# Kernel tuning notes

Measured on AMD Instinct MI355X. Metric: run time of the kernel, lower is better.

Reference implementation:

```python
import jax, jax.numpy as jnp
import numpy as np

S, B, H, F, E, K = 2048, 4, 1024, 4096, 8, 2


def setup_inputs() -> dict:
    key = jax.random.key(0)
    k1, k2, k3, k4 = jax.random.split(key, 4)
    scale_h = 1.0 / np.sqrt(H)
    scale_f = 1.0 / np.sqrt(F)
    return {
        "x": jax.random.normal(k1, (S, B, H), dtype=jnp.float32),
        "router_w": jax.random.normal(k2, (H, E), dtype=jnp.float32) * scale_h,
        "w1": jax.random.normal(k3, (E, H, F), dtype=jnp.float32) * scale_h,
        "w2": jax.random.normal(k4, (E, F, H), dtype=jnp.float32) * scale_f,
    }


def reference(x, router_w, w1, w2):
    # x: [S, B, H] (Megatron layout). Flatten to tokens.
    s, b, h = x.shape
    xt = x.reshape(-1, h)                       # [T, H], T = S*B
    # --- TopK router: softmax over expert logits, then top-k probs ---
    logits = xt @ router_w                      # [T, E]
    probs = jax.nn.softmax(logits, axis=-1)     # [T, E]
    top_p, top_i = jax.lax.top_k(probs, K)      # [T, K] each
    # --- Grouped-GEMM expert MLPs + weighted combine ---
    # Loop over the small fixed expert set; each expert applies fc1->gelu->fc2
    # to every token, masked/weighted by its routing probability (math is
    # identical to dispatch/permute/grouped-GEMM/combine in Megatron).
    out = jnp.zeros_like(xt)
    for e in range(E):
        gate_e = jnp.sum(jnp.where(top_i == e, top_p, 0.0), axis=-1)  # [T]
        hidden = jax.nn.gelu(xt @ w1[e], approximate=True)            # [T, F]
        out = out + gate_e[:, None] * (hidden @ w2[e])                # [T, H]
    return out.reshape(s, b, h)
```

## Files before the change

kernel.cpp:

```cpp
#include <hip/hip_runtime.h>
#include <cstdint>
#include <cstddef>

#define T_TOKENS 8192
#define H_DIM    1024
#define F_DIM    4096
#define E_NUM    8

typedef __bf16 bf16x8 __attribute__((ext_vector_type(8)));
typedef float  f32x4  __attribute__((ext_vector_type(4)));
typedef unsigned short ushort8 __attribute__((ext_vector_type(8)));

#define AS_GLOBAL(p) ((const __attribute__((address_space(1))) void*)(p))
#define AS_LDS(p)    ((__attribute__((address_space(3))) void*)(p))

__device__ inline unsigned short f2b(float f) {
  unsigned int u = __float_as_uint(f);
  unsigned int r = (u + 0x7fffu + ((u >> 16) & 1u)) >> 16;
  return (unsigned short)r;
}
__device__ inline float b2f(unsigned short u) {
  return __uint_as_float(((unsigned int)u) << 16);
}
__device__ inline float gelu_fast(float v) {
  float u2 = 1.5957691216057308f * v * (1.0f + 0.044715f * v * v);
  return v / (1.0f + __expf(-u2));
}

__global__ __launch_bounds__(256) void transpose_cast_kernel(
    const float* __restrict__ in, unsigned short* __restrict__ out, int R, int C,
    int* __restrict__ zc)
{
  __shared__ float tile[64][65];
  const int tid = threadIdx.x;
  if (zc && blockIdx.x == 0 && blockIdx.y == 0 && blockIdx.z == 0 && tid < 24)
    zc[tid] = 0;
  const int e  = blockIdx.z;
  const int c0 = blockIdx.x * 64;
  const int r0 = blockIdx.y * 64;
  const float* src = in + (size_t)e * R * C;
  unsigned short* dst = out + (size_t)e * R * C;
  const int rl  = tid >> 4;
  const int cl4 = (tid & 15) * 4;
#pragma unroll
  for (int i = 0; i < 4; ++i) {
    float4 v = *(const float4*)(src + (size_t)(r0 + rl + i * 16) * C + c0 + cl4);
    tile[rl + i * 16][cl4 + 0] = v.x;
    tile[rl + i * 16][cl4 + 1] = v.y;
    tile[rl + i * 16][cl4 + 2] = v.z;
    tile[rl + i * 16][cl4 + 3] = v.w;
  }
  __syncthreads();
#pragma unroll
  for (int itw = 0; itw < 2; ++itw) {
    int g  = itw * 256 + tid;
    int c  = g >> 3;
    int rc = g & 7;
    ushort8 u;
#pragma unroll
    for (int k = 0; k < 8; ++k) u[k] = f2b(tile[rc * 8 + k][c]);
    *(ushort8*)(dst + (size_t)(c0 + c) * R + r0 + rc * 8) = u;
  }
}

__global__ __launch_bounds__(256) void router_kernel(
    const float* __restrict__ x, const float* __restrict__ rw,
    unsigned short* __restrict__ xb, int* __restrict__ top_e, float* __restrict__ top_p,
    int* __restrict__ counts, float* __restrict__ out_zero)
{
  __shared__ float lrw[H_DIM * 9];
  __shared__ int lc[E_NUM];
  const int tid = threadIdx.x;
  {
    float4 z = {0.f, 0.f, 0.f, 0.f};
    float4* o4 = (float4*)out_zero;
    int base = blockIdx.x * 256 + tid;
#pragma unroll
    for (int i = 0; i < 32; ++i) o4[base + i * 65536] = z;
  }
  if (tid < E_NUM) lc[tid] = 0;
  for (int r = tid; r < H_DIM; r += 256) {
    const float* s = rw + r * 8;
    float4 a = *(const float4*)(s);
    float4 b = *(const float4*)(s + 4);
    float* d = &lrw[r * 9];
    d[0] = a.x; d[1] = a.y; d[2] = a.z; d[3] = a.w;
    d[4] = b.x; d[5] = b.y; d[6] = b.z; d[7] = b.w;
  }
  __syncthreads();
  const int lane = tid & 63, wid = tid >> 6;
  for (int i = 0; i < 8; ++i) {
    const int t = blockIdx.x * 32 + wid * 8 + i;
    float acc[8] = {0.f, 0.f, 0.f, 0.f, 0.f, 0.f, 0.f, 0.f};
    const float* xrow = x + (size_t)t * H_DIM;
    unsigned short* xbrow = xb + (size_t)t * H_DIM;
#pragma unroll
    for (int j = 0; j < 16; ++j) {
      int h = j * 64 + lane;
      float xv = xrow[h];
      xbrow[h] = f2b(xv);
      const float* rr = &lrw[h * 9];
#pragma unroll
      for (int e = 0; e < 8; ++e) acc[e] += xv * rr[e];
    }
#pragma unroll
    for (int e = 0; e < 8; ++e) {
#pragma unroll
      for (int s = 32; s > 0; s >>= 1) acc[e] += __shfl_xor(acc[e], s, 64);
    }
    if (lane == 0) {
      float mx = acc[0];
      for (int e = 1; e < 8; ++e) mx = fmaxf(mx, acc[e]);
      float p[8]; float sum = 0.f;
      for (int e = 0; e < 8; ++e) { p[e] = expf(acc[e] - mx); sum += p[e]; }
      float inv = 1.0f / sum;
      int i1 = 0; float b1 = p[0];
      for (int e = 1; e < 8; ++e) if (p[e] > b1) { b1 = p[e]; i1 = e; }
      int i2 = (i1 == 0) ? 1 : 0; float b2 = p[i2];
      for (int e = 0; e < 8; ++e) if (e != i1 && p[e] > b2) { b2 = p[e]; i2 = e; }
      top_e[2 * t]     = i1; top_p[2 * t]     = b1 * inv;
      top_e[2 * t + 1] = i2; top_p[2 * t + 1] = b2 * inv;
      atomicAdd(&lc[i1], 1);
      atomicAdd(&lc[i2], 1);
    }
  }
  __syncthreads();
  if (tid < E_NUM) atomicAdd(&counts[tid], lc[tid]);
}

__global__ __launch_bounds__(256) void assign_kernel(
    const int* __restrict__ top_e, const float* __restrict__ top_p,
    const int* __restrict__ counts, int* __restrict__ cursor,
    int* __restrict__ map, float* __restrict__ gate, int* __restrict__ offsets)
{
  __shared__ int lc[E_NUM], lb[E_NUM], loff[E_NUM];
  const int tid = threadIdx.x;
  const int t = blockIdx.x * 256 + tid;
  if (tid < E_NUM) lc[tid] = 0;
  if (tid == 0) {
    int o = 0;
    for (int e = 0; e < E_NUM; ++e) { loff[e] = o; o += counts[e]; }
  }
  __syncthreads();
  int e0 = top_e[2 * t], e1 = top_e[2 * t + 1];
  int p0 = atomicAdd(&lc[e0], 1);
  int p1 = atomicAdd(&lc[e1], 1);
  __syncthreads();
  if (tid < E_NUM) lb[tid] = atomicAdd(&cursor[tid], lc[tid]);
  __syncthreads();
  int s0 = loff[e0] + lb[e0] + p0;
  int s1 = loff[e1] + lb[e1] + p1;
  map[s0] = t; gate[s0] = top_p[2 * t];
  map[s1] = t; gate[s1] = top_p[2 * t + 1];
  if (blockIdx.x == 0 && tid < E_NUM) offsets[tid] = loff[tid];
}

template <int KD, int ND, bool USE_MAP, bool GELU, bool ATOMIC_OUT>
__global__ __launch_bounds__(256) void moe_gemm_kernel(
    const unsigned short* __restrict__ A, const unsigned short* __restrict__ Bt,
    const int* __restrict__ map, const float* __restrict__ gate,
    const int* __restrict__ counts, const int* __restrict__ offsets,
    unsigned short* __restrict__ C, float* __restrict__ out)
{
  __shared__ unsigned short ls[32768];
  const int e   = blockIdx.x;
  const int cnt = counts[e];
  const int tile_m = blockIdx.y;
  if (tile_m * 128 >= cnt) return;
  const int off    = offsets[e];
  const int tile_n = blockIdx.z;
  const int tid    = threadIdx.x;

  const unsigned short* aSrc[4];
  const unsigned short* bSrc[4];
  const int cswz = ((tid & 7) ^ ((tid >> 3) & 7)) * 8;
#pragma unroll
  for (int it = 0; it < 4; ++it) {
    int r  = it * 32 + (tid >> 3);
    int rm = tile_m * 128 + r;
    if (rm > cnt - 1) rm = cnt - 1;
    int arow = USE_MAP ? map[off + rm] : (off + rm);
    aSrc[it] = A + (size_t)arow * KD + cswz;
    int rn = tile_n * 128 + r;
    bSrc[it] = Bt + (size_t)e * ND * KD + (size_t)rn * KD + cswz;
  }

  const int lane = tid & 63;
  const int wid  = tid >> 6;
  const int wm = wid >> 1, wn = wid & 1;
  const int lr = lane & 15, kg = lane >> 4;
  const int swz = lr & 7;

  f32x4 acc[4][4];
#pragma unroll
  for (int mi = 0; mi < 4; ++mi)
#pragma unroll
    for (int ni = 0; ni < 4; ++ni) acc[mi][ni] = (f32x4){0.f, 0.f, 0.f, 0.f};

  constexpr int NK = KD / 64;

#pragma unroll
  for (int it = 0; it < 4; ++it)
    __builtin_amdgcn_global_load_lds(AS_GLOBAL(aSrc[it]),
                                     AS_LDS(ls + (it * 256 + tid) * 8), 16, 0, 0);
#pragma unroll
  for (int it = 0; it < 4; ++it)
    __builtin_amdgcn_global_load_lds(AS_GLOBAL(bSrc[it]),
                                     AS_LDS(ls + 16384 + (it * 256 + tid) * 8), 16, 0, 0);

#pragma unroll 1
  for (int k = 0; k < NK; ++k) {
    const int p = k & 1;
    asm volatile("s_barrier" ::: "memory");
    if (k + 1 < NK) {
      const int q = p ^ 1;
      const int k0 = (k + 1) * 64;
#pragma unroll
      for (int it = 0; it < 4; ++it)
        __builtin_amdgcn_global_load_lds(AS_GLOBAL(aSrc[it] + k0),
                                         AS_LDS(ls + q * 8192 + (it * 256 + tid) * 8), 16, 0, 0);
#pragma unroll
      for (int it = 0; it < 4; ++it)
        __builtin_amdgcn_global_load_lds(AS_GLOBAL(bSrc[it] + k0),
                                         AS_LDS(ls + 16384 + q * 8192 + (it * 256 + tid) * 8), 16, 0, 0);
      asm volatile("s_waitcnt vmcnt(8)" ::: "memory");
    } else {
      asm volatile("s_waitcnt vmcnt(0)" ::: "memory");
    }
    asm volatile("s_barrier" ::: "memory");

    const unsigned short* pA = ls + p * 8192 + (wm * 64 + lr) * 64;
    const unsigned short* pB = ls + 16384 + p * 8192 + (wn * 64 + lr) * 64;
#pragma unroll
    for (int ks = 0; ks < 2; ++ks) {
      bf16x8 aF[4], bF[4];
#pragma unroll
      for (int i = 0; i < 4; ++i)
        aF[i] = *(const bf16x8*)(pA + i * 16 * 64 + (((ks * 4 + kg) ^ swz) * 8));
#pragma unroll
      for (int i = 0; i < 4; ++i)
        bF[i] = *(const bf16x8*)(pB + i * 16 * 64 + (((ks * 4 + kg) ^ swz) * 8));
#pragma unroll
      for (int mi = 0; mi < 4; ++mi)
#pragma unroll
        for (int ni = 0; ni < 4; ++ni)
          acc[mi][ni] = __builtin_amdgcn_mfma_f32_16x16x32_bf16(aF[mi], bF[ni],
                                                                acc[mi][ni], 0, 0, 0);
    }
  }

  if (ATOMIC_OUT) {
#pragma unroll
    for (int mi = 0; mi < 4; ++mi) {
#pragma unroll
      for (int r = 0; r < 4; ++r) {
        int Rl = wm * 64 + mi * 16 + kg * 4 + r;
        int gm = tile_m * 128 + Rl;
        if (gm < cnt) {
          int   t  = map[off + gm];
          float gv = gate[off + gm];
          float* orow = out + (size_t)t * ND + tile_n * 128 + wn * 64 + lr;
#pragma unroll
          for (int ni = 0; ni < 4; ++ni)
            __hip_atomic_fetch_add(orow + ni * 16, acc[mi][ni][r] * gv,
                                   __ATOMIC_RELAXED, __HIP_MEMORY_SCOPE_AGENT);
        }
      }
    }
  } else {
    __syncthreads();
#pragma unroll
    for (int mi = 0; mi < 4; ++mi) {
#pragma unroll
      for (int r = 0; r < 4; ++r) {
        int Rl = wm * 64 + mi * 16 + kg * 4 + r;
#pragma unroll
        for (int ni = 0; ni < 4; ++ni) {
          int col = wn * 64 + ni * 16 + lr;
          float v = acc[mi][ni][r];
          v = GELU ? gelu_fast(v) : v;
          ls[Rl * 136 + col] = f2b(v);
        }
      }
    }
    __syncthreads();
#pragma unroll
    for (int it = 0; it < 8; ++it) {
      int g = it * 256 + tid;
      int R = g >> 4, c16 = g & 15;
      int gm = tile_m * 128 + R;
      if (gm < cnt) {
        ushort8 v = *(const ushort8*)(ls + R * 136 + c16 * 8);
        *(ushort8*)(C + (size_t)(off + gm) * ND + tile_n * 128 + c16 * 8) = v;
      }
    }
  }
}

extern "C" void kernel_launch(void* const* d_in, const int* in_sizes, int n_in,
                              void* d_out, int out_size, void* d_ws, size_t ws_size,
                              hipStream_t stream) {
  const float* x  = (const float*)d_in[0];
  const float* rw = (const float*)d_in[1];
  const float* w1 = (const float*)d_in[2];
  const float* w2 = (const float*)d_in[3];
  float* out = (float*)d_out;

  char* ws = (char*)d_ws;
  unsigned short* wT     = (unsigned short*)ws;
  unsigned short* xb     = (unsigned short*)(ws + (64ull  << 20));
  unsigned short* hidden = (unsigned short*)(ws + (96ull  << 20));
  char* meta = ws + (224ull << 20);
  int*   top_e   = (int*)meta;
  float* top_p   = (float*)(meta + (64 << 10));
  int*   map     = (int*)(meta + (128 << 10));
  float* gate    = (float*)(meta + (192 << 10));
  int*   counts  = (int*)(meta + (320 << 10));
  int*   offsets = counts + 8;
  int*   cursor  = counts + 16;

  transpose_cast_kernel<<<dim3(F_DIM / 64, H_DIM / 64, E_NUM), 256, 0, stream>>>(
      w1, wT, H_DIM, F_DIM, counts);
  router_kernel<<<256, 256, 0, stream>>>(x, rw, xb, top_e, top_p, counts, out);
  assign_kernel<<<T_TOKENS / 256, 256, 0, stream>>>(top_e, top_p, counts, cursor,
                                                    map, gate, offsets);
  moe_gemm_kernel<H_DIM, F_DIM, true, true, false>
      <<<dim3(E_NUM, 64, F_DIM / 128), 256, 0, stream>>>(xb, wT, map, gate,
                                                         counts, offsets, hidden, nullptr);
  transpose_cast_kernel<<<dim3(H_DIM / 64, F_DIM / 64, E_NUM), 256, 0, stream>>>(
      w2, wT, F_DIM, H_DIM, nullptr);
  moe_gemm_kernel<F_DIM, H_DIM, false, false, true>
      <<<dim3(E_NUM, 64, H_DIM / 128), 256, 0, stream>>>(hidden, wT, map, gate,
                                                         counts, offsets, nullptr, out);
}
```

Measured before the change: 765.1 us.

## Add 256x256-tile triple-buffered GEMM kernel for the fc1 expert stage

Adds a new grouped-GEMM kernel for fc1 that uses 512-thread blocks computing 256x256 output tiles with a k-step of 32. It keeps three LDS buffers filled through global_load_lds and splits the A/B staging between two MFMA phases, which raise wave priority via setprio. The aim is more data reuse per block and better overlap of loads with MFMA work than the older 128x128 kernel. The cost is 96KB of LDS and larger accumulator register use per block, which lowers occupancy and may leave tiles partly empty when an expert has few tokens.

```diff
diff --git a/kernel.cpp b/kernel.cpp
--- a/kernel.cpp
+++ b/kernel.cpp
@@ -155,6 +155,153 @@
   if (blockIdx.x == 0 && tid < E_NUM) offsets[tid] = loff[tid];
 }
 
+template <int KD, int ND, bool USE_MAP, bool GELU>
+__global__ __launch_bounds__(512, 2) void moe_gemm_k32_kernel(
+    const unsigned short* __restrict__ A, const unsigned short* __restrict__ Bt,
+    const int* __restrict__ map, const float* __restrict__ gate,
+    const int* __restrict__ counts, const int* __restrict__ offsets,
+    unsigned short* __restrict__ C)
+{
+  __shared__ unsigned short ls[49152];
+  const int e   = blockIdx.x;
+  const int cnt = counts[e];
+  const int tile_m = blockIdx.y;
+  if (tile_m * 256 >= cnt) return;
+  const int off    = offsets[e];
+  const int tile_n = blockIdx.z;
+  const int tid    = threadIdx.x;
+
+  const unsigned short* aSrc[2];
+  const unsigned short* bSrc[2];
+#pragma unroll
+  for (int it = 0; it < 2; ++it) {
+    int g   = it * 512 + tid;
+    int row = g >> 2;
+    int cs  = (g & 3) ^ (row & 3);
+    int rm  = tile_m * 256 + row;
+    if (rm > cnt - 1) rm = cnt - 1;
+    int arow = USE_MAP ? map[off + rm] : (off + rm);
+    aSrc[it] = A + (size_t)arow * KD + cs * 8;
+    int rn = tile_n * 256 + row;
+    bSrc[it] = Bt + (size_t)e * ND * KD + (size_t)rn * KD + cs * 8;
+  }
+
+  const int lane = tid & 63;
+  const int wid  = tid >> 6;
+  const int wm = wid >> 2, wn = wid & 3;
+  const int lr = lane & 15, kg = lane >> 4;
+  const int kc = ((kg ^ (lr & 3)) * 8);
+
+  f32x4 acc[8][4];
+#pragma unroll
+  for (int mi = 0; mi < 8; ++mi)
+#pragma unroll
+    for (int ni = 0; ni < 4; ++ni) acc[mi][ni] = (f32x4){0.f, 0.f, 0.f, 0.f};
+
+  constexpr int NK = KD / 32;
+
+  auto STAGE_A = [&](int kt, int slot) {
+    const int kof = kt * 32;
+#pragma unroll
+    for (int it = 0; it < 2; ++it)
+      __builtin_amdgcn_global_load_lds(AS_GLOBAL(aSrc[it] + kof),
+          AS_LDS(ls + slot * 8192 + (it * 512 + tid) * 8), 16, 0, 0);
+  };
+  auto STAGE_B = [&](int kt, int slot) {
+    const int kof = kt * 32;
+#pragma unroll
+    for (int it = 0; it < 2; ++it)
+      __builtin_amdgcn_global_load_lds(AS_GLOBAL(bSrc[it] + kof),
+          AS_LDS(ls + 24576 + slot * 8192 + (it * 512 + tid) * 8), 16, 0, 0);
+  };
+
+  STAGE_A(0, 0); STAGE_B(0, 0);
+  STAGE_A(1, 1); STAGE_B(1, 1);
+  asm volatile("s_waitcnt vmcnt(4)" ::: "memory");
+  asm volatile("s_barrier" ::: "memory");
+
+  int sc = 0;
+  int st = 2;
+#pragma unroll 1
+  for (int kt = 0; kt < NK; ++kt) {
+    const bool stg = (kt + 2 < NK);
+    const unsigned short* pA = ls + sc * 8192 + (wm * 128 + lr) * 32;
+    const unsigned short* pB = ls + 24576 + sc * 8192 + (wn * 64 + lr) * 32;
+    bf16x8 aF[4], bF[4];
+
+#pragma unroll
+    for (int ni = 0; ni < 4; ++ni)
+      bF[ni] = *(const bf16x8*)(pB + ni * 16 * 32 + kc);
+#pragma unroll
+    for (int j = 0; j < 4; ++j)
+      aF[j] = *(const bf16x8*)(pA + j * 16 * 32 + kc);
+    if (stg) STAGE_A(kt + 2, st);
+    asm volatile("s_barrier" ::: "memory");
+    __builtin_amdgcn_s_setprio(1);
+#pragma unroll
+    for (int j = 0; j < 4; ++j)
+#pragma unroll
+      for (int ni = 0; ni < 4; ++ni)
+        acc[j][ni] = __builtin_amdgcn_mfma_f32_16x16x32_bf16(aF[j], bF[ni], acc[j][ni], 0, 0, 0);
+    __builtin_amdgcn_s_setprio(0);
+    asm volatile("s_barrier" ::: "memory");
+
+#pragma unroll
+    for (int j = 0; j < 4; ++j)
+      aF[j] = *(const bf16x8*)(pA + (4 + j) * 16 * 32 + kc);
+    if (stg) STAGE_B(kt + 2, st);
+    asm volatile("s_barrier" ::: "memory");
+    __builtin_amdgcn_s_setprio(1);
+#pragma unroll
+    for (int j = 0; j < 4; ++j)
+#pragma unroll
+      for (int ni = 0; ni < 4; ++ni)
+        acc[4 + j][ni] = __builtin_amdgcn_mfma_f32_16x16x32_bf16(aF[j], bF[ni], acc[4 + j][ni], 0, 0, 0);
+    __builtin_amdgcn_s_setprio(0);
+    if (stg) {
+      asm volatile("s_waitcnt vmcnt(4)" ::: "memory");
+    } else if (kt + 1 < NK) {
+      asm volatile("s_waitcnt vmcnt(0)" ::: "memory");
+    }
+    asm volatile("s_barrier" ::: "memory");
+    sc = (sc == 2) ? 0 : sc + 1;
+    st = (st == 2) ? 0 : st + 1;
+  }
+
+  __syncthreads();
+#pragma unroll
+  for (int h = 0; h < 2; ++h) {
+    if (h) __syncthreads();
+    if (wm == h) {
+#pragma unroll
+      for (int mi = 0; mi < 8; ++mi) {
+#pragma unroll
+        for (int r = 0; r < 4; ++r) {
+          int Rl = mi * 16 + kg * 4 + r;
+#pragma unroll
+          for (int ni = 0; ni < 4; ++ni) {
+            int col = wn * 64 + ni * 16 + lr;
+            float v = acc[mi][ni][r];
+            v = GELU ? gelu_fast(v) : v;
+            ls[Rl * 264 + col] = f2b(v);
+          }
+        }
+      }
+    }
+    __syncthreads();
+#pragma unroll
+    for (int it = 0; it < 8; ++it) {
+      int g = it * 512 + tid;
+      int R = g >> 5, c8 = g & 31;
+      int gm = tile_m * 256 + h * 128 + R;
+      if (gm < cnt) {
+        ushort8 v = *(const ushort8*)(ls + R * 264 + c8 * 8);
+        *(ushort8*)(C + (size_t)(off + gm) * ND + tile_n * 256 + c8 * 8) = v;
+      }
+    }
+  }
+}
+
 template <int KD, int ND, bool USE_MAP, bool GELU, bool ATOMIC_OUT>
 __global__ __launch_bounds__(256) void moe_gemm_kernel(
     const unsigned short* __restrict__ A, const unsigned short* __restrict__ Bt,
@@ -324,9 +471,9 @@
   router_kernel<<<256, 256, 0, stream>>>(x, rw, xb, top_e, top_p, counts, out);
   assign_kernel<<<T_TOKENS / 256, 256, 0, stream>>>(top_e, top_p, counts, cursor,
                                                     map, gate, offsets);
-  moe_gemm_kernel<H_DIM, F_DIM, true, true, false>
-      <<<dim3(E_NUM, 64, F_DIM / 128), 256, 0, stream>>>(xb, wT, map, gate,
-                                                         counts, offsets, hidden, nullptr);
+  moe_gemm_k32_kernel<H_DIM, F_DIM, true, true>
+      <<<dim3(E_NUM, 32, F_DIM / 256), 512, 0, stream>>>(xb, wT, map, gate,
+                                                         counts, offsets, hidden);
   transpose_cast_kernel<<<dim3(H_DIM / 64, F_DIM / 64, E_NUM), 256, 0, stream>>>(
       w2, wT, F_DIM, H_DIM, nullptr);
   moe_gemm_kernel<F_DIM, H_DIM, false, false, true>
```

Result: slower. 826.1 us (+8.0%).

## Replace atomic scatter-add combine with per-slot gated output and gather combine

Applied to the files above, without the earlier changes.

The second expert GEMM now writes gate-weighted results as bf16 rows per routed slot instead of doing fp32 atomic adds into the output. A new combine kernel gathers each token's two slot rows via a slot_of index built in the assign kernel and writes the fp32 sum, so the output zeroing in the router is dropped. This removes contended global atomics and the zero-fill pass. In exchange it adds an extra kernel and an intermediate buffer, and rounds per-expert contributions to bf16 before summing.

```diff
diff --git a/kernel.cpp b/kernel.cpp
--- a/kernel.cpp
+++ b/kernel.cpp
@@ -66,18 +66,11 @@
 __global__ __launch_bounds__(256) void router_kernel(
     const float* __restrict__ x, const float* __restrict__ rw,
     unsigned short* __restrict__ xb, int* __restrict__ top_e, float* __restrict__ top_p,
-    int* __restrict__ counts, float* __restrict__ out_zero)
+    int* __restrict__ counts)
 {
   __shared__ float lrw[H_DIM * 9];
   __shared__ int lc[E_NUM];
   const int tid = threadIdx.x;
-  {
-    float4 z = {0.f, 0.f, 0.f, 0.f};
-    float4* o4 = (float4*)out_zero;
-    int base = blockIdx.x * 256 + tid;
-#pragma unroll
-    for (int i = 0; i < 32; ++i) o4[base + i * 65536] = z;
-  }
   if (tid < E_NUM) lc[tid] = 0;
   for (int r = tid; r < H_DIM; r += 256) {
     const float* s = rw + r * 8;
@@ -131,7 +124,8 @@
 __global__ __launch_bounds__(256) void assign_kernel(
     const int* __restrict__ top_e, const float* __restrict__ top_p,
     const int* __restrict__ counts, int* __restrict__ cursor,
-    int* __restrict__ map, float* __restrict__ gate, int* __restrict__ offsets)
+    int* __restrict__ map, float* __restrict__ gate, int* __restrict__ slot_of,
+    int* __restrict__ offsets)
 {
   __shared__ int lc[E_NUM], lb[E_NUM], loff[E_NUM];
   const int tid = threadIdx.x;
@@ -152,15 +146,16 @@
   int s1 = loff[e1] + lb[e1] + p1;
   map[s0] = t; gate[s0] = top_p[2 * t];
   map[s1] = t; gate[s1] = top_p[2 * t + 1];
+  slot_of[2 * t] = s0; slot_of[2 * t + 1] = s1;
   if (blockIdx.x == 0 && tid < E_NUM) offsets[tid] = loff[tid];
 }
 
-template <int KD, int ND, bool USE_MAP, bool GELU, bool ATOMIC_OUT>
+template <int KD, int ND, bool USE_MAP>
 __global__ __launch_bounds__(256) void moe_gemm_kernel(
     const unsigned short* __restrict__ A, const unsigned short* __restrict__ Bt,
-    const int* __restrict__ map, const float* __restrict__ gate,
+    const int* __restrict__ map,
     const int* __restrict__ counts, const int* __restrict__ offsets,
-    unsigned short* __restrict__ C, float* __restrict__ out)
+    unsigned short* __restrict__ C)
 {
   __shared__ unsigned short ls[32768];
   const int e   = blockIdx.x;
@@ -249,52 +244,169 @@
     }
   }
 
-  if (ATOMIC_OUT) {
-#pragma unroll
-    for (int mi = 0; mi < 4; ++mi) {
-#pragma unroll
-      for (int r = 0; r < 4; ++r) {
-        int Rl = wm * 64 + mi * 16 + kg * 4 + r;
-        int gm = tile_m * 128 + Rl;
-        if (gm < cnt) {
-          int   t  = map[off + gm];
-          float gv = gate[off + gm];
-          float* orow = out + (size_t)t * ND + tile_n * 128 + wn * 64 + lr;
-#pragma unroll
-          for (int ni = 0; ni < 4; ++ni)
-            __hip_atomic_fetch_add(orow + ni * 16, acc[mi][ni][r] * gv,
-                                   __ATOMIC_RELAXED, __HIP_MEMORY_SCOPE_AGENT);
-        }
+  __syncthreads();
+#pragma unroll
+  for (int mi = 0; mi < 4; ++mi) {
+#pragma unroll
+    for (int r = 0; r < 4; ++r) {
+      int Rl = wm * 64 + mi * 16 + kg * 4 + r;
+#pragma unroll
+      for (int ni = 0; ni < 4; ++ni) {
+        int col = wn * 64 + ni * 16 + lr;
+        ls[Rl * 136 + col] = f2b(gelu_fast(acc[mi][ni][r]));
       }
     }
-  } else {
-    __syncthreads();
-#pragma unroll
-    for (int mi = 0; mi < 4; ++mi) {
-#pragma unroll
-      for (int r = 0; r < 4; ++r) {
-        int Rl = wm * 64 + mi * 16 + kg * 4 + r;
-#pragma unroll
-        for (int ni = 0; ni < 4; ++ni) {
-          int col = wn * 64 + ni * 16 + lr;
-          float v = acc[mi][ni][r];
-          v = GELU ? gelu_fast(v) : v;
-          ls[Rl * 136 + col] = f2b(v);
-        }
+  }
+  __syncthreads();
+#pragma unroll
+  for (int it = 0; it < 8; ++it) {
+    int g = it * 256 + tid;
+    int R = g >> 4, c16 = g & 15;
+    int gm = tile_m * 128 + R;
+    if (gm < cnt) {
+      ushort8 v = *(const ushort8*)(ls + R * 136 + c16 * 8);
+      *(ushort8*)(C + (size_t)(off + gm) * ND + tile_n * 128 + c16 * 8) = v;
+    }
+  }
+}
+
+template <int KD, int ND>
+__global__ __launch_bounds__(256) void moe_gemm_fc2_kernel(
+    const unsigned short* __restrict__ A, const unsigned short* __restrict__ Bt,
+    const float* __restrict__ gate,
+    const int* __restrict__ counts, const int* __restrict__ offsets,
+    unsigned short* __restrict__ C)
+{
+  __shared__ unsigned short ls[32768];
+  const int e   = blockIdx.x;
+  const int cnt = counts[e];
+  const int tile_m = blockIdx.y;
+  if (tile_m * 128 >= cnt) return;
+  const int off    = offsets[e];
+  const int tile_n = blockIdx.z;
+  const int tid    = threadIdx.x;
+
+  const unsigned short* aSrc[4];
+  const unsigned short* bSrc[4];
+  const int cswz = ((tid & 7) ^ ((tid >> 3) & 7)) * 8;
+#pragma unroll
+  for (int it = 0; it < 4; ++it) {
+    int r  = it * 32 + (tid >> 3);
+    int rm = tile_m * 128 + r;
+    if (rm > cnt - 1) rm = cnt - 1;
+    aSrc[it] = A + (size_t)(off + rm) * KD + cswz;
+    int rn = tile_n * 128 + r;
+    bSrc[it] = Bt + (size_t)e * ND * KD + (size_t)rn * KD + cswz;
+  }
+
+  const int lane = tid & 63;
+  const int wid  = tid >> 6;
+  const int wm = wid >> 1, wn = wid & 1;
+  const int lr = lane & 15, kg = lane >> 4;
+  const int swz = lr & 7;
+
+  f32x4 acc[4][4];
+#pragma unroll
+  for (int mi = 0; mi < 4; ++mi)
+#pragma unroll
+    for (int ni = 0; ni < 4; ++ni) acc[mi][ni] = (f32x4){0.f, 0.f, 0.f, 0.f};
+
+  constexpr int NK = KD / 64;
+
+#pragma unroll
+  for (int it = 0; it < 4; ++it)
+    __builtin_amdgcn_global_load_lds(AS_GLOBAL(aSrc[it]),
+                                     AS_LDS(ls + (it * 256 + tid) * 8), 16, 0, 0);
+#pragma unroll
+  for (int it = 0; it < 4; ++it)
+    __builtin_amdgcn_global_load_lds(AS_GLOBAL(bSrc[it]),
+                                     AS_LDS(ls + 16384 + (it * 256 + tid) * 8), 16, 0, 0);
+
+#pragma unroll 1
+  for (int k = 0; k < NK; ++k) {
+    const int p = k & 1;
+    asm volatile("s_barrier" ::: "memory");
+    if (k + 1 < NK) {
+      const int q = p ^ 1;
+      const int k0 = (k + 1) * 64;
+#pragma unroll
+      for (int it = 0; it < 4; ++it)
+        __builtin_amdgcn_global_load_lds(AS_GLOBAL(aSrc[it] + k0),
+                                         AS_LDS(ls + q * 8192 + (it * 256 + tid) * 8), 16, 0, 0);
+#pragma unroll
+      for (int it = 0; it < 4; ++it)
+        __builtin_amdgcn_global_load_lds(AS_GLOBAL(bSrc[it] + k0),
+                                         AS_LDS(ls + 16384 + q * 8192 + (it * 256 + tid) * 8), 16, 0, 0);
+      asm volatile("s_waitcnt vmcnt(8)" ::: "memory");
+    } else {
+      asm volatile("s_waitcnt vmcnt(0)" ::: "memory");
+    }
+    asm volatile("s_barrier" ::: "memory");
+
+    const unsigned short* pA = ls + p * 8192 + (wm * 64 + lr) * 64;
+    const unsigned short* pB = ls + 16384 + p * 8192 + (wn * 64 + lr) * 64;
+#pragma unroll
+    for (int ks = 0; ks < 2; ++ks) {
+      bf16x8 aF[4], bF[4];
+#pragma unroll
+      for (int i = 0; i < 4; ++i)
+        aF[i] = *(const bf16x8*)(pA + i * 16 * 64 + (((ks * 4 + kg) ^ swz) * 8));
+#pragma unroll
+      for (int i = 0; i < 4; ++i)
+        bF[i] = *(const bf16x8*)(pB + i * 16 * 64 + (((ks * 4 + kg) ^ swz) * 8));
+#pragma unroll
+      for (int mi = 0; mi < 4; ++mi)
+#pragma unroll
+        for (int ni = 0; ni < 4; ++ni)
+          acc[mi][ni] = __builtin_amdgcn_mfma_f32_16x16x32_bf16(aF[mi], bF[ni],
+                                                                acc[mi][ni], 0, 0, 0);
+    }
+  }
+
+  __syncthreads();
+#pragma unroll
+  for (int mi = 0; mi < 4; ++mi) {
+#pragma unroll
+    for (int r = 0; r < 4; ++r) {
+      int Rl = wm * 64 + mi * 16 + kg * 4 + r;
+      int gm = tile_m * 128 + Rl;
+      int gmc = gm < cnt ? gm : cnt - 1;
+      float gv = gate[off + gmc];
+#pragma unroll
+      for (int ni = 0; ni < 4; ++ni) {
+        int col = wn * 64 + ni * 16 + lr;
+        ls[Rl * 136 + col] = f2b(acc[mi][ni][r] * gv);
       }
     }
-    __syncthreads();
-#pragma unroll
-    for (int it = 0; it < 8; ++it) {
-      int g = it * 256 + tid;
-      int R = g >> 4, c16 = g & 15;
-      int gm = tile_m * 128 + R;
-      if (gm < cnt) {
-        ushort8 v = *(const ushort8*)(ls + R * 136 + c16 * 8);
-        *(ushort8*)(C + (size_t)(off + gm) * ND + tile_n * 128 + c16 * 8) = v;
-      }
-    }
-  }
+  }
+  __syncthreads();
+#pragma unroll
+  for (int it = 0; it < 8; ++it) {
+    int g = it * 256 + tid;
+    int R = g >> 4, c16 = g & 15;
+    int gm = tile_m * 128 + R;
+    if (gm < cnt) {
+      ushort8 v = *(const ushort8*)(ls + R * 136 + c16 * 8);
+      *(ushort8*)(C + (size_t)(off + gm) * ND + tile_n * 128 + c16 * 8) = v;
+    }
+  }
+}
+
+__global__ __launch_bounds__(256) void combine_kernel(
+    const unsigned short* __restrict__ y, const int* __restrict__ slot_of,
+    float* __restrict__ out)
+{
+  const int t  = blockIdx.x;
+  const int h0 = threadIdx.x * 4;
+  const int s0 = slot_of[2 * t], s1 = slot_of[2 * t + 1];
+  ushort4 a = *(const ushort4*)(y + (size_t)s0 * H_DIM + h0);
+  ushort4 b = *(const ushort4*)(y + (size_t)s1 * H_DIM + h0);
+  float4 o;
+  o.x = b2f(a.x) + b2f(b.x);
+  o.y = b2f(a.y) + b2f(b.y);
+  o.z = b2f(a.z) + b2f(b.z);
+  o.w = b2f(a.w) + b2f(b.w);
+  *(float4*)(out + (size_t)t * H_DIM + h0) = o;
 }
 
 extern "C" void kernel_launch(void* const* d_in, const int* in_sizes, int n_in,
@@ -309,27 +421,30 @@
   char* ws = (char*)d_ws;
   unsigned short* wT     = (unsigned short*)ws;
   unsigned short* xb     = (unsigned short*)(ws + (64ull  << 20));
+  unsigned short* y      = (unsigned short*)(ws + (64ull  << 20));
   unsigned short* hidden = (unsigned short*)(ws + (96ull  << 20));
   char* meta = ws + (224ull << 20);
   int*   top_e   = (int*)meta;
   float* top_p   = (float*)(meta + (64 << 10));
   int*   map     = (int*)(meta + (128 << 10));
   float* gate    = (float*)(meta + (192 << 10));
+  int*   slot_of = (int*)(meta + (256 << 10));
   int*   counts  = (int*)(meta + (320 << 10));
   int*   offsets = counts + 8;
   int*   cursor  = counts + 16;
 
   transpose_cast_kernel<<<dim3(F_DIM / 64, H_DIM / 64, E_NUM), 256, 0, stream>>>(
       w1, wT, H_DIM, F_DIM, counts);
-  router_kernel<<<256, 256, 0, stream>>>(x, rw, xb, top_e, top_p, counts, out);
+  router_kernel<<<256, 256, 0, stream>>>(x, rw, xb, top_e, top_p, counts);
   assign_kernel<<<T_TOKENS / 256, 256, 0, stream>>>(top_e, top_p, counts, cursor,
-                                                    map, gate, offsets);
-  moe_gemm_kernel<H_DIM, F_DIM, true, true, false>
-      <<<dim3(E_NUM, 64, F_DIM / 128), 256, 0, stream>>>(xb, wT, map, gate,
-                                                         counts, offsets, hidden, nullptr);
+                                                    map, gate, slot_of, offsets);
+  moe_gemm_kernel<H_DIM, F_DIM, true>
+      <<<dim3(E_NUM, 64, F_DIM / 128), 256, 0, stream>>>(xb, wT, map,
+                                                         counts, offsets, hidden);
   transpose_cast_kernel<<<dim3(H_DIM / 64, F_DIM / 64, E_NUM), 256, 0, stream>>>(
       w2, wT, F_DIM, H_DIM, nullptr);
-  moe_gemm_kernel<F_DIM, H_DIM, false, false, true>
-      <<<dim3(E_NUM, 64, H_DIM / 128), 256, 0, stream>>>(hidden, wT, map, gate,
-                                                         counts, offsets, nullptr, out);
-}
+  moe_gemm_fc2_kernel<F_DIM, H_DIM>
+      <<<dim3(E_NUM, 64, H_DIM / 128), 256, 0, stream>>>(hidden, wT, gate,
+                                                         counts, offsets, y);
+  combine_kernel<<<T_TOKENS, 256, 0, stream>>>(y, slot_of, out);
+}
```

Measured after the change: 740.5 us. 1.03x faster.

## Use 256x256 GEMM tiles with finer pipeline and replace atomic scatter with combine

Applied to the files above, without the earlier changes.

Both expert GEMMs move from 128x128 tiles on 256 threads to 256x256 tiles on 512 threads. Each 64-wide k step is split into two 32-wide half-stages across a four-slot LDS ring, with setprio around the MFMA bursts to overlap loads with compute. The second GEMM now writes gated bf16 results into a per-slot buffer instead of doing fp32 atomics into the output. A new combine kernel sums each token's two slots, which also removes the output zeroing. The bigger tiles mean more M-padding waste for experts with uneven counts, more register pressure, and a bf16 rounding of the fc2 output before the sum.

```diff
diff --git a/kernel.cpp b/kernel.cpp
--- a/kernel.cpp
+++ b/kernel.cpp
@@ -66,18 +66,11 @@
 __global__ __launch_bounds__(256) void router_kernel(
     const float* __restrict__ x, const float* __restrict__ rw,
     unsigned short* __restrict__ xb, int* __restrict__ top_e, float* __restrict__ top_p,
-    int* __restrict__ counts, float* __restrict__ out_zero)
+    int* __restrict__ counts)
 {
   __shared__ float lrw[H_DIM * 9];
   __shared__ int lc[E_NUM];
   const int tid = threadIdx.x;
-  {
-    float4 z = {0.f, 0.f, 0.f, 0.f};
-    float4* o4 = (float4*)out_zero;
-    int base = blockIdx.x * 256 + tid;
-#pragma unroll
-    for (int i = 0; i < 32; ++i) o4[base + i * 65536] = z;
-  }
   if (tid < E_NUM) lc[tid] = 0;
   for (int r = tid; r < H_DIM; r += 256) {
     const float* s = rw + r * 8;
@@ -131,7 +124,8 @@
 __global__ __launch_bounds__(256) void assign_kernel(
     const int* __restrict__ top_e, const float* __restrict__ top_p,
     const int* __restrict__ counts, int* __restrict__ cursor,
-    int* __restrict__ map, float* __restrict__ gate, int* __restrict__ offsets)
+    int* __restrict__ map, float* __restrict__ gate, int* __restrict__ slot_of,
+    int* __restrict__ offsets)
 {
   __shared__ int lc[E_NUM], lb[E_NUM], loff[E_NUM];
   const int tid = threadIdx.x;
@@ -152,149 +146,197 @@
   int s1 = loff[e1] + lb[e1] + p1;
   map[s0] = t; gate[s0] = top_p[2 * t];
   map[s1] = t; gate[s1] = top_p[2 * t + 1];
+  slot_of[2 * t] = s0; slot_of[2 * t + 1] = s1;
   if (blockIdx.x == 0 && tid < E_NUM) offsets[tid] = loff[tid];
 }
 
-template <int KD, int ND, bool USE_MAP, bool GELU, bool ATOMIC_OUT>
-__global__ __launch_bounds__(256) void moe_gemm_kernel(
+template <int KD, int ND, bool USE_MAP, bool GELU>
+__global__ __launch_bounds__(512, 2) void moe_gemm256_kernel(
     const unsigned short* __restrict__ A, const unsigned short* __restrict__ Bt,
     const int* __restrict__ map, const float* __restrict__ gate,
     const int* __restrict__ counts, const int* __restrict__ offsets,
-    unsigned short* __restrict__ C, float* __restrict__ out)
-{
-  __shared__ unsigned short ls[32768];
+    unsigned short* __restrict__ C)
+{
+  __shared__ unsigned short ls[65536];
   const int e   = blockIdx.x;
   const int cnt = counts[e];
   const int tile_m = blockIdx.y;
-  if (tile_m * 128 >= cnt) return;
+  if (tile_m * 256 >= cnt) return;
   const int off    = offsets[e];
   const int tile_n = blockIdx.z;
   const int tid    = threadIdx.x;
 
-  const unsigned short* aSrc[4];
-  const unsigned short* bSrc[4];
-  const int cswz = ((tid & 7) ^ ((tid >> 3) & 7)) * 8;
-#pragma unroll
-  for (int it = 0; it < 4; ++it) {
-    int r  = it * 32 + (tid >> 3);
-    int rm = tile_m * 128 + r;
-    if (rm > cnt - 1) rm = cnt - 1;
-    int arow = USE_MAP ? map[off + rm] : (off + rm);
-    aSrc[it] = A + (size_t)arow * KD + cswz;
-    int rn = tile_n * 128 + r;
-    bSrc[it] = Bt + (size_t)e * ND * KD + (size_t)rn * KD + cswz;
-  }
+  const int row_lo = tid >> 2;
+  const int kcl8 = (((tid & 3) ^ (row_lo & 3)) * 8);
+  int rm0 = tile_m * 256 + row_lo;        if (rm0 > cnt - 1) rm0 = cnt - 1;
+  int rm1 = tile_m * 256 + row_lo + 128;  if (rm1 > cnt - 1) rm1 = cnt - 1;
+  const int ar0 = USE_MAP ? map[off + rm0] : (off + rm0);
+  const int ar1 = USE_MAP ? map[off + rm1] : (off + rm1);
+  const unsigned short* aP0 = A + (size_t)ar0 * KD + kcl8;
+  const unsigned short* aP1 = A + (size_t)ar1 * KD + kcl8;
+  const unsigned short* bBase = Bt + (size_t)e * ND * KD;
+  const unsigned short* bP0 = bBase + (size_t)(tile_n * 256 + row_lo) * KD + kcl8;
+  const unsigned short* bP1 = bBase + (size_t)(tile_n * 256 + row_lo + 128) * KD + kcl8;
+
+  auto STAGE_A = [&](int k, int h) {
+    const int ko = k * 64 + h * 32;
+    const int sl = (2 * k + h) & 3;
+    __builtin_amdgcn_global_load_lds(AS_GLOBAL(aP0 + ko),
+        AS_LDS(ls + sl * 8192 + tid * 8), 16, 0, 0);
+    __builtin_amdgcn_global_load_lds(AS_GLOBAL(aP1 + ko),
+        AS_LDS(ls + sl * 8192 + (512 + tid) * 8), 16, 0, 0);
+  };
+  auto STAGE_B = [&](int k, int h) {
+    const int ko = k * 64 + h * 32;
+    const int sl = (2 * k + h) & 3;
+    __builtin_amdgcn_global_load_lds(AS_GLOBAL(bP0 + ko),
+        AS_LDS(ls + 32768 + sl * 8192 + tid * 8), 16, 0, 0);
+    __builtin_amdgcn_global_load_lds(AS_GLOBAL(bP1 + ko),
+        AS_LDS(ls + 32768 + sl * 8192 + (512 + tid) * 8), 16, 0, 0);
+  };
 
   const int lane = tid & 63;
   const int wid  = tid >> 6;
-  const int wm = wid >> 1, wn = wid & 1;
+  const int wm = wid >> 2, wn = wid & 3;
   const int lr = lane & 15, kg = lane >> 4;
-  const int swz = lr & 7;
-
-  f32x4 acc[4][4];
-#pragma unroll
-  for (int mi = 0; mi < 4; ++mi)
+  const int kx8 = ((kg ^ (lr & 3)) * 8);
+  const int aRd = (wm * 128 + lr) * 32 + kx8;
+  const int bRd = (wn * 64  + lr) * 32 + kx8;
+
+  f32x4 acc[8][4];
+#pragma unroll
+  for (int mi = 0; mi < 8; ++mi)
 #pragma unroll
     for (int ni = 0; ni < 4; ++ni) acc[mi][ni] = (f32x4){0.f, 0.f, 0.f, 0.f};
 
   constexpr int NK = KD / 64;
 
-#pragma unroll
-  for (int it = 0; it < 4; ++it)
-    __builtin_amdgcn_global_load_lds(AS_GLOBAL(aSrc[it]),
-                                     AS_LDS(ls + (it * 256 + tid) * 8), 16, 0, 0);
-#pragma unroll
-  for (int it = 0; it < 4; ++it)
-    __builtin_amdgcn_global_load_lds(AS_GLOBAL(bSrc[it]),
-                                     AS_LDS(ls + 16384 + (it * 256 + tid) * 8), 16, 0, 0);
+  STAGE_A(0, 0); STAGE_B(0, 0); STAGE_A(0, 1); STAGE_B(0, 1);
+  STAGE_A(1, 0); STAGE_B(1, 0);
+  asm volatile("s_waitcnt vmcnt(4)" ::: "memory");
+  asm volatile("s_barrier" ::: "memory");
 
 #pragma unroll 1
   for (int k = 0; k < NK; ++k) {
-    const int p = k & 1;
+    const unsigned short* pA0 = ls + (((2 * k) & 3) * 8192) + aRd;
+    const unsigned short* pB0 = ls + 32768 + (((2 * k) & 3) * 8192) + bRd;
+    const unsigned short* pA1 = ls + (((2 * k + 1) & 3) * 8192) + aRd;
+    const unsigned short* pB1 = ls + 32768 + (((2 * k + 1) & 3) * 8192) + bRd;
+    bf16x8 aF[4], bF[4];
+
+#pragma unroll
+    for (int ni = 0; ni < 4; ++ni) bF[ni] = *(const bf16x8*)(pB0 + ni * 512);
+#pragma unroll
+    for (int j = 0; j < 4; ++j)    aF[j]  = *(const bf16x8*)(pA0 + j * 512);
+    if (k + 1 < NK) STAGE_A(k + 1, 1);
+    __builtin_amdgcn_s_setprio(1);
+#pragma unroll
+    for (int j = 0; j < 4; ++j)
+#pragma unroll
+      for (int ni = 0; ni < 4; ++ni)
+        acc[j][ni] = __builtin_amdgcn_mfma_f32_16x16x32_bf16(aF[j], bF[ni], acc[j][ni], 0, 0, 0);
+    __builtin_amdgcn_s_setprio(0);
     asm volatile("s_barrier" ::: "memory");
-    if (k + 1 < NK) {
-      const int q = p ^ 1;
-      const int k0 = (k + 1) * 64;
-#pragma unroll
-      for (int it = 0; it < 4; ++it)
-        __builtin_amdgcn_global_load_lds(AS_GLOBAL(aSrc[it] + k0),
-                                         AS_LDS(ls + q * 8192 + (it * 256 + tid) * 8), 16, 0, 0);
-#pragma unroll
-      for (int it = 0; it < 4; ++it)
-        __builtin_amdgcn_global_load_lds(AS_GLOBAL(bSrc[it] + k0),
-                                         AS_LDS(ls + 16384 + q * 8192 + (it * 256 + tid) * 8), 16, 0, 0);
-      asm volatile("s_waitcnt vmcnt(8)" ::: "memory");
+
+#pragma unroll
+    for (int j = 0; j < 4; ++j)    aF[j] = *(const bf16x8*)(pA0 + (4 + j) * 512);
+    if (k + 1 < NK) STAGE_B(k + 1, 1);
+    __builtin_amdgcn_s_setprio(1);
+#pragma unroll
+    for (int j = 0; j < 4; ++j)
+#pragma unroll
+      for (int ni = 0; ni < 4; ++ni)
+        acc[4 + j][ni] = __builtin_amdgcn_mfma_f32_16x16x32_bf16(aF[j], bF[ni], acc[4 + j][ni], 0, 0, 0);
+    __builtin_amdgcn_s_setprio(0);
+    asm volatile("s_barrier" ::: "memory");
+
+#pragma unroll
+    for (int ni = 0; ni < 4; ++ni) bF[ni] = *(const bf16x8*)(pB1 + ni * 512);
+#pragma unroll
+    for (int j = 0; j < 4; ++j)    aF[j]  = *(const bf16x8*)(pA1 + j * 512);
+    if (k + 2 < NK) STAGE_A(k + 2, 0);
+    __builtin_amdgcn_s_setprio(1);
+#pragma unroll
+    for (int j = 0; j < 4; ++j)
+#pragma unroll
+      for (int ni = 0; ni < 4; ++ni)
+        acc[j][ni] = __builtin_amdgcn_mfma_f32_16x16x32_bf16(aF[j], bF[ni], acc[j][ni], 0, 0, 0);
+    __builtin_amdgcn_s_setprio(0);
+    asm volatile("s_barrier" ::: "memory");
+
+#pragma unroll
+    for (int j = 0; j < 4; ++j)    aF[j] = *(const bf16x8*)(pA1 + (4 + j) * 512);
+    if (k + 2 < NK) STAGE_B(k + 2, 0);
+    __builtin_amdgcn_s_setprio(1);
+#pragma unroll
+    for (int j = 0; j < 4; ++j)
+#pragma unroll
+      for (int ni = 0; ni < 4; ++ni)
+        acc[4 + j][ni] = __builtin_amdgcn_mfma_f32_16x16x32_bf16(aF[j], bF[ni], acc[4 + j][ni], 0, 0, 0);
+    __builtin_amdgcn_s_setprio(0);
+    if (k >= NK - 2) {
+      asm volatile("s_waitcnt vmcnt(0)" ::: "memory");
     } else {
-      asm volatile("s_waitcnt vmcnt(0)" ::: "memory");
+      asm volatile("s_waitcnt vmcnt(4)" ::: "memory");
     }
     asm volatile("s_barrier" ::: "memory");
-
-    const unsigned short* pA = ls + p * 8192 + (wm * 64 + lr) * 64;
-    const unsigned short* pB = ls + 16384 + p * 8192 + (wn * 64 + lr) * 64;
-#pragma unroll
-    for (int ks = 0; ks < 2; ++ks) {
-      bf16x8 aF[4], bF[4];
-#pragma unroll
-      for (int i = 0; i < 4; ++i)
-        aF[i] = *(const bf16x8*)(pA + i * 16 * 64 + (((ks * 4 + kg) ^ swz) * 8));
-#pragma unroll
-      for (int i = 0; i < 4; ++i)
-        bF[i] = *(const bf16x8*)(pB + i * 16 * 64 + (((ks * 4 + kg) ^ swz) * 8));
-#pragma unroll
-      for (int mi = 0; mi < 4; ++mi)
-#pragma unroll
-        for (int ni = 0; ni < 4; ++ni)
-          acc[mi][ni] = __builtin_amdgcn_mfma_f32_16x16x32_bf16(aF[mi], bF[ni],
-                                                                acc[mi][ni], 0, 0, 0);
-    }
-  }
-
-  if (ATOMIC_OUT) {
-#pragma unroll
-    for (int mi = 0; mi < 4; ++mi) {
-#pragma unroll
-      for (int r = 0; r < 4; ++r) {
-        int Rl = wm * 64 + mi * 16 + kg * 4 + r;
-        int gm = tile_m * 128 + Rl;
-        if (gm < cnt) {
-          int   t  = map[off + gm];
-          float gv = gate[off + gm];
-          float* orow = out + (size_t)t * ND + tile_n * 128 + wn * 64 + lr;
-#pragma unroll
-          for (int ni = 0; ni < 4; ++ni)
-            __hip_atomic_fetch_add(orow + ni * 16, acc[mi][ni][r] * gv,
-                                   __ATOMIC_RELAXED, __HIP_MEMORY_SCOPE_AGENT);
+  }
+
+  __syncthreads();
+#pragma unroll
+  for (int h = 0; h < 2; ++h) {
+    if (h) __syncthreads();
+    if (wm == h) {
+#pragma unroll
+      for (int mi = 0; mi < 8; ++mi) {
+#pragma unroll
+        for (int r = 0; r < 4; ++r) {
+          int Rl = mi * 16 + kg * 4 + r;
+          float gv = 1.0f;
+          if (!GELU) {
+            int gm = tile_m * 256 + h * 128 + Rl;
+            int gmc = gm < cnt ? gm : cnt - 1;
+            gv = gate[off + gmc];
+          }
+#pragma unroll
+          for (int ni = 0; ni < 4; ++ni) {
+            int col = wn * 64 + ni * 16 + lr;
+            float v = acc[mi][ni][r];
+            v = GELU ? gelu_fast(v) : v * gv;
+            ls[Rl * 264 + col] = f2b(v);
+          }
         }
       }
     }
-  } else {
     __syncthreads();
 #pragma unroll
-    for (int mi = 0; mi < 4; ++mi) {
-#pragma unroll
-      for (int r = 0; r < 4; ++r) {
-        int Rl = wm * 64 + mi * 16 + kg * 4 + r;
-#pragma unroll
-        for (int ni = 0; ni < 4; ++ni) {
-          int col = wn * 64 + ni * 16 + lr;
-          float v = acc[mi][ni][r];
-          v = GELU ? gelu_fast(v) : v;
-          ls[Rl * 136 + col] = f2b(v);
-        }
+    for (int it = 0; it < 8; ++it) {
+      int g = it * 512 + tid;
+      int R = g >> 5, c8 = g & 31;
+      int gm = tile_m * 256 + h * 128 + R;
+      if (gm < cnt) {
+        ushort8 v = *(const ushort8*)(ls + R * 264 + c8 * 8);
+        *(ushort8*)(C + (size_t)(off + gm) * ND + tile_n * 256 + c8 * 8) = v;
       }
     }
-    __syncthreads();
-#pragma unroll
-    for (int it = 0; it < 8; ++it) {
-      int g = it * 256 + tid;
-      int R = g >> 4, c16 = g & 15;
-      int gm = tile_m * 128 + R;
-      if (gm < cnt) {
-        ushort8 v = *(const ushort8*)(ls + R * 136 + c16 * 8);
-        *(ushort8*)(C + (size_t)(off + gm) * ND + tile_n * 128 + c16 * 8) = v;
-      }
-    }
-  }
+  }
+}
+
+__global__ __launch_bounds__(256) void combine_kernel(
+    const unsigned short* __restrict__ y, const int* __restrict__ slot_of,
+    float* __restrict__ out)
+{
+  const int t  = blockIdx.x;
+  const int h0 = threadIdx.x * 4;
+  const int s0 = slot_of[2 * t], s1 = slot_of[2 * t + 1];
+  ushort4 a = *(const ushort4*)(y + (size_t)s0 * H_DIM + h0);
+  ushort4 b = *(const ushort4*)(y + (size_t)s1 * H_DIM + h0);
+  float4 o;
+  o.x = b2f(a.x) + b2f(b.x);
+  o.y = b2f(a.y) + b2f(b.y);
+  o.z = b2f(a.z) + b2f(b.z);
+  o.w = b2f(a.w) + b2f(b.w);
+  *(float4*)(out + (size_t)t * H_DIM + h0) = o;
 }
 
 extern "C" void kernel_launch(void* const* d_in, const int* in_sizes, int n_in,
@@ -309,27 +351,30 @@
   char* ws = (char*)d_ws;
   unsigned short* wT     = (unsigned short*)ws;
   unsigned short* xb     = (unsigned short*)(ws + (64ull  << 20));
+  unsigned short* y      = (unsigned short*)(ws + (64ull  << 20));
   unsigned short* hidden = (unsigned short*)(ws + (96ull  << 20));
   char* meta = ws + (224ull << 20);
   int*   top_e   = (int*)meta;
   float* top_p   = (float*)(meta + (64 << 10));
   int*   map     = (int*)(meta + (128 << 10));
   float* gate    = (float*)(meta + (192 << 10));
+  int*   slot_of = (int*)(meta + (256 << 10));
   int*   counts  = (int*)(meta + (320 << 10));
   int*   offsets = counts + 8;
   int*   cursor  = counts + 16;
 
   transpose_cast_kernel<<<dim3(F_DIM / 64, H_DIM / 64, E_NUM), 256, 0, stream>>>(
       w1, wT, H_DIM, F_DIM, counts);
-  router_kernel<<<256, 256, 0, stream>>>(x, rw, xb, top_e, top_p, counts, out);
+  router_kernel<<<256, 256, 0, stream>>>(x, rw, xb, top_e, top_p, counts);
   assign_kernel<<<T_TOKENS / 256, 256, 0, stream>>>(top_e, top_p, counts, cursor,
-                                                    map, gate, offsets);
-  moe_gemm_kernel<H_DIM, F_DIM, true, true, false>
-      <<<dim3(E_NUM, 64, F_DIM / 128), 256, 0, stream>>>(xb, wT, map, gate,
-                                                         counts, offsets, hidden, nullptr);
+                                                    map, gate, slot_of, offsets);
+  moe_gemm256_kernel<H_DIM, F_DIM, true, true>
+      <<<dim3(E_NUM, 32, F_DIM / 256), 512, 0, stream>>>(xb, wT, map, nullptr,
+                                                         counts, offsets, hidden);
   transpose_cast_kernel<<<dim3(H_DIM / 64, F_DIM / 64, E_NUM), 256, 0, stream>>>(
       w2, wT, F_DIM, H_DIM, nullptr);
-  moe_gemm_kernel<F_DIM, H_DIM, false, false, true>
-      <<<dim3(E_NUM, 64, H_DIM / 128), 256, 0, stream>>>(hidden, wT, map, gate,
-                                                         counts, offsets, nullptr, out);
-}
+  moe_gemm256_kernel<F_DIM, H_DIM, false, false>
+      <<<dim3(E_NUM, 32, H_DIM / 256), 512, 0, stream>>>(hidden, wT, nullptr, gate,
+                                                         counts, offsets, y);
+  combine_kernel<<<T_TOKENS, 256, 0, stream>>>(y, slot_of, out);
+}
```

Measured after the change: 823.4 us. 7.6% more time.
